# Optimization experiments

Hardware: AMD Instinct MI355X
Metric: run time of the kernel (lower is better)

The kernel has to match this reference:

```python
import jax, jax.numpy as jnp
import numpy as np

N_EMBD = 1024
N_HEAD = 16
HEAD_DIM = N_EMBD // N_HEAD


def setup_inputs() -> dict:
    key = jax.random.key(0)
    k1, k2, k3, k4, k5 = jax.random.split(key, 5)
    B, T, C = 4, 2048, N_EMBD
    s = 1.0 / np.sqrt(C)
    return {
        "x": jax.random.normal(k1, (B, T, C), dtype=jnp.float32),
        "W_attn": jax.random.normal(k2, (C, 3 * C), dtype=jnp.float32) * s,
        "b_attn": jnp.zeros((3 * C,), dtype=jnp.float32),
        "W_proj": jax.random.normal(k3, (C, C), dtype=jnp.float32) * s,
        "b_proj": jnp.zeros((C,), dtype=jnp.float32),
    }


def reference(x, W_attn, b_attn, W_proj, b_proj):
    B, T, C = x.shape
    H, D = N_HEAD, HEAD_DIM
    # fused QKV projection
    qkv = x @ W_attn + b_attn                       # [B,T,3C]
    q, k, v = jnp.split(qkv, 3, axis=2)
    q = q.reshape(B, T, H, D).transpose(0, 2, 1, 3)  # [B,H,T,D]
    k = k.reshape(B, T, H, D).transpose(0, 2, 1, 3)
    v = v.reshape(B, T, H, D).transpose(0, 2, 1, 3)
    # causal scaled dot-product attention
    scale = 1.0 / jnp.sqrt(jnp.asarray(D, dtype=x.dtype))
    scores = jnp.einsum('bhqd,bhkd->bhqk', q, k) * scale  # [B,H,T,T]
    causal = jnp.tril(jnp.ones((T, T), dtype=bool))
    scores = jnp.where(causal[None, None], scores, jnp.finfo(x.dtype).min)
    attn = jax.nn.softmax(scores, axis=-1)
    y = jnp.einsum('bhqk,bhkd->bhqd', attn, v)      # [B,H,T,D]
    y = y.transpose(0, 2, 1, 3).reshape(B, T, C)
    return y @ W_proj + b_proj
```

## Files before the change

kernel.cpp:

```cpp
#include <hip/hip_runtime.h>
#include <hip/hip_bf16.h>
#include <cstdint>

#define B_ 4
#define T_ 2048
#define C_ 1024
#define H_ 16
#define D_ 64
#define M_ (B_*T_)
#define N3 (3*C_)

typedef __bf16 bf16;
typedef __bf16 bf16x8 __attribute__((ext_vector_type(8)));
typedef __bf16 bf16x4 __attribute__((ext_vector_type(4)));
typedef float  floatx4 __attribute__((ext_vector_type(4)));

__device__ __forceinline__ void gl_lds16(const bf16* g, bf16* l) {
  __builtin_amdgcn_global_load_lds(
      (__attribute__((address_space(1))) void*)(void*)g,
      (__attribute__((address_space(3))) void*)(void*)l,
      16, 0, 0);
}

__device__ __forceinline__ uint32_t pack_bf16_trunc(float lo, float hi) {
  union { float f; uint32_t u; } a, b;
  a.f = lo; b.f = hi;
  return (a.u >> 16) | (b.u & 0xffff0000u);
}

__global__ void cast_to_bf16(const float* __restrict__ in, bf16* __restrict__ out, int n) {
  int i = (blockIdx.x * blockDim.x + threadIdx.x) * 4;
  if (i < n) {
    const float4 f = *(const float4*)(in + i);
    bf16x4 o;
    o.x = (bf16)f.x; o.y = (bf16)f.y; o.z = (bf16)f.z; o.w = (bf16)f.w;
    *(bf16x4*)(out + i) = o;
  }
}

__global__ void transpose_cast(const float* __restrict__ in, bf16* __restrict__ out,
                               int R, int C) {
  __shared__ float tile[32][33];
  int r0 = blockIdx.y * 32, c0 = blockIdx.x * 32;
  int tx = threadIdx.x & 31, ty = threadIdx.x >> 5;
  #pragma unroll
  for (int j = 0; j < 32; j += 8)
    tile[ty + j][tx] = in[(size_t)(r0 + ty + j) * C + c0 + tx];
  __syncthreads();
  #pragma unroll
  for (int j = 0; j < 32; j += 8)
    out[(size_t)(c0 + ty + j) * R + r0 + tx] = (bf16)tile[tx][ty + j];
}

__global__ __launch_bounds__(256)
void transpose_v(const bf16* __restrict__ in, bf16* __restrict__ out) {
  __shared__ __attribute__((aligned(16))) bf16 tileN[64 * 64];
  const int tid = threadIdx.x;
  const int bh = blockIdx.z;
  const int t0 = blockIdx.x * 64;
  const int sk = tid >> 2, scc = tid & 3;
  {
    const bf16* p = in + ((size_t)bh * T_ + t0 + sk) * D_ + scc * 16;
    const bf16x8 r0 = *(const bf16x8*)p;
    const bf16x8 r1 = *(const bf16x8*)(p + 8);
    *(bf16x8*)(tileN + sk * 64 + ((2 * scc)     ^ (sk & 7)) * 8) = r0;
    *(bf16x8*)(tileN + sk * 64 + ((2 * scc + 1) ^ (sk & 7)) * 8) = r1;
  }
  __syncthreads();
  const int tc = (tid & 7) * 8;
  #pragma unroll
  for (int half = 0; half < 2; half++) {
    const int d = (tid >> 3) + half * 32;
    bf16x8 o;
    #pragma unroll
    for (int j = 0; j < 8; j++) {
      const int slot = tc + j;
      const int row = 16 * (slot & 3) + (slot >> 2);
      o[j] = tileN[row * 64 + (((d >> 3) ^ (row & 7)) * 8) + (d & 7)];
    }
    *(bf16x8*)(out + ((size_t)bh * D_ + d) * T_ + t0 + tc) = o;
  }
}

template<int MODE>
__global__ __launch_bounds__(256)
void gemm_bt(const bf16* __restrict__ A, const bf16* __restrict__ Bt,
             const float* __restrict__ bias, float* __restrict__ out,
             bf16* __restrict__ qo, bf16* __restrict__ ko, bf16* __restrict__ vo,
             int M, int N, int K)
{
  __shared__ __attribute__((aligned(16))) bf16 As[128 * 32];
  __shared__ __attribute__((aligned(16))) bf16 Bs[128 * 32];

  const int tid  = threadIdx.x;
  const int w    = tid >> 6;
  const int lane = tid & 63;
  const int quad = lane >> 4;
  const int l16  = lane & 15;
  const int wm   = w & 1, wn = w >> 1;
  const int m0   = blockIdx.y * 128, n0 = blockIdx.x * 128;

  floatx4 acc[4][4] = {};

  const int lrow = lane >> 2;
  const int lk   = (lane & 3) * 8;

  const bf16* aptr = A  + (size_t)(m0 + w * 32 + lrow) * K + lk;
  const bf16* bptr = Bt + (size_t)(n0 + w * 32 + lrow) * K + lk;
  bf16* asl = As + w * 1024;
  bf16* bsl = Bs + w * 1024;

  for (int k0 = 0; k0 < K; k0 += 32) {
    gl_lds16(aptr,          asl);
    gl_lds16(aptr + 16 * K, asl + 512);
    gl_lds16(bptr,          bsl);
    gl_lds16(bptr + 16 * K, bsl + 512);
    aptr += 32; bptr += 32;
    __syncthreads();

    bf16x8 af[4], bfb[4];
    #pragma unroll
    for (int i = 0; i < 4; i++)
      af[i] = *(const bf16x8*)(As + (wm * 64 + i * 16 + l16) * 32 + quad * 8);
    #pragma unroll
    for (int i = 0; i < 4; i++)
      bfb[i] = *(const bf16x8*)(Bs + (wn * 64 + i * 16 + l16) * 32 + quad * 8);
    #pragma unroll
    for (int mi = 0; mi < 4; mi++)
      #pragma unroll
      for (int ni = 0; ni < 4; ni++)
        acc[mi][ni] = __builtin_amdgcn_mfma_f32_16x16x32_bf16(af[mi], bfb[ni], acc[mi][ni], 0, 0, 0);
    __syncthreads();
  }

  #pragma unroll
  for (int mi = 0; mi < 4; mi++) {
    #pragma unroll
    for (int ni = 0; ni < 4; ni++) {
      const int col = n0 + wn * 64 + ni * 16 + l16;
      const float bv = bias[col];
      #pragma unroll
      for (int r = 0; r < 4; r++) {
        const int row = m0 + wm * 64 + mi * 16 + quad * 4 + r;
        const float val = acc[mi][ni][r] + bv;
        if (MODE == 0) {
          const int b = row >> 11, t = row & 2047;
          const int s = col >> 10, c = col & 1023;
          const int h = c >> 6,  d = c & 63;
          bf16* dst = (s == 0) ? qo : (s == 1) ? ko : vo;
          dst[((size_t)(b * H_ + h) * T_ + t) * D_ + d] = (bf16)val;
        } else {
          out[(size_t)row * N + col] = val;
        }
      }
    }
  }
}


__device__ __forceinline__ void stage8(const bf16* g, int K, bf16* lds, int lane) {
  const int r = lane >> 3, s = (lane & 7) ^ r;
  gl_lds16(g + (size_t)r * K + s * 8, lds);
}
__device__ __forceinline__ void stage_half(const bf16* g, int K, bf16* lds, int wv, int lane) {
  stage8(g + (size_t)(wv * 16) * K,     K, lds + (wv * 16) * 64, lane);
  stage8(g + (size_t)(wv * 16 + 8) * K, K, lds + (wv * 16 + 8) * 64, lane);
}

#define GBAR asm volatile("s_barrier" ::: "memory")

template<int MODE>
__global__ __launch_bounds__(512, 2)
void gemm256(const bf16* __restrict__ A, const bf16* __restrict__ Bt,
             const float* __restrict__ bias, float* __restrict__ out,
             bf16* __restrict__ qo, bf16* __restrict__ ko, bf16* __restrict__ vo,
             int M, int N, int K)
{
  __shared__ __attribute__((aligned(16))) bf16 As[2][256 * 64];
  __shared__ __attribute__((aligned(16))) bf16 Bs[2][256 * 64];

  const int tid  = threadIdx.x;
  const int wv   = tid >> 6, lane = tid & 63;
  const int quad = lane >> 4, l16 = lane & 15;
  const int wm   = wv >> 2, wn = wv & 3;
  const int n0   = blockIdx.x * 256, m0 = blockIdx.y * 256;
  const int NTT  = K >> 6;

  floatx4 acc[8][4] = {};

  const bf16* Abase = A  + (size_t)m0 * K;
  const bf16* Bbase = Bt + (size_t)n0 * K;

  stage_half(Abase,                  K, As[0],            wv, lane);
  stage_half(Abase + (size_t)128*K,  K, As[0] + 128 * 64, wv, lane);
  stage_half(Bbase,                  K, Bs[0],            wv, lane);
  stage_half(Bbase + (size_t)128*K,  K, Bs[0] + 128 * 64, wv, lane);
  stage_half(Bbase + 64,             K, Bs[1],            wv, lane);
  stage_half(Abase + 64,             K, As[1],            wv, lane);
  asm volatile("s_waitcnt vmcnt(4)" ::: "memory");
  GBAR;

#define LOADA(qm)                                                          \
  _Pragma("unroll")                                                        \
  for (int mi = 0; mi < 4; mi++) {                                         \
    const int row = wm * 128 + (qm) * 64 + mi * 16 + l16;                  \
    const bf16* rp = bufA + row * 64;                                      \
    af[mi][0] = *(const bf16x8*)(rp + (( quad      ^ (row & 7)) * 8));     \
    af[mi][1] = *(const bf16x8*)(rp + (((4 | quad) ^ (row & 7)) * 8));     \
  }
#define LOADB(qn)                                                          \
  _Pragma("unroll")                                                        \
  for (int ni = 0; ni < 2; ni++) {                                         \
    const int row = wn * 64 + (qn) * 32 + ni * 16 + l16;                   \
    const bf16* rp = bufB + row * 64;                                      \
    bfr[(qn)*2+ni][0] = *(const bf16x8*)(rp + (( quad      ^ (row & 7)) * 8)); \
    bfr[(qn)*2+ni][1] = *(const bf16x8*)(rp + (((4 | quad) ^ (row & 7)) * 8)); \
  }
#define MM(qm, qn)                                                         \
  __builtin_amdgcn_s_setprio(1);                                           \
  _Pragma("unroll")                                                        \
  for (int mi = 0; mi < 4; mi++)                                           \
    _Pragma("unroll")                                                      \
    for (int ni = 0; ni < 2; ni++) {                                       \
      acc[(qm)*4+mi][(qn)*2+ni] = __builtin_amdgcn_mfma_f32_16x16x32_bf16( \
          af[mi][0], bfr[(qn)*2+ni][0], acc[(qm)*4+mi][(qn)*2+ni], 0, 0, 0); \
      acc[(qm)*4+mi][(qn)*2+ni] = __builtin_amdgcn_mfma_f32_16x16x32_bf16( \
          af[mi][1], bfr[(qn)*2+ni][1], acc[(qm)*4+mi][(qn)*2+ni], 0, 0, 0); \
    }                                                                      \
  __builtin_amdgcn_s_setprio(0);

  #pragma unroll 1
  for (int t = 0; t < NTT; t++) {
    const int cur = t & 1;
    const bf16* bufA = As[cur];
    const bf16* bufB = Bs[cur];
    bf16* nA = As[cur ^ 1];
    bf16* nB = Bs[cur ^ 1];
    bf16* cA = As[cur];
    bf16* cB = Bs[cur];
    const int kn1 = (t + 1) * 64, kn2 = (t + 2) * 64;
    const bool h1 = (t + 1 < NTT), h2 = (t + 2 < NTT);

    bf16x8 af[4][2], bfr[4][2];

    LOADA(0);
    LOADB(0);
    if (h1) stage_half(Abase + (size_t)128 * K + kn1, K, nA + 128 * 64, wv, lane);
    GBAR;
    MM(0, 0);
    GBAR;

    LOADB(1);
    if (h1) stage_half(Bbase + (size_t)128 * K + kn1, K, nB + 128 * 64, wv, lane);
    GBAR;
    MM(0, 1);
    GBAR;

    LOADA(1);
    if (h2) stage_half(Bbase + kn2, K, cB, wv, lane);
    GBAR;
    MM(1, 0);
    GBAR;

    if (h2) stage_half(Abase + kn2, K, cA, wv, lane);
    GBAR;
    MM(1, 1);
    asm volatile("s_waitcnt vmcnt(4)" ::: "memory");
    GBAR;
  }

#undef LOADA
#undef LOADB
#undef MM

  #pragma unroll
  for (int mi8 = 0; mi8 < 8; mi8++) {
    #pragma unroll
    for (int nf = 0; nf < 4; nf++) {
      const int col = n0 + wn * 64 + nf * 16 + l16;
      const float bv = bias[col];
      #pragma unroll
      for (int r = 0; r < 4; r++) {
        const int row = m0 + wm * 128 + mi8 * 16 + quad * 4 + r;
        const float val = acc[mi8][nf][r] + bv;
        if (MODE == 0) {
          const int b = row >> 11, tt = row & 2047;
          const int s = col >> 10, c = col & 1023;
          const int h = c >> 6, d = c & 63;
          bf16* dst = (s == 0) ? qo : (s == 1) ? ko : vo;
          dst[((size_t)(b * H_ + h) * T_ + tt) * D_ + d] = (bf16)val;
        } else {
          out[(size_t)row * N + col] = val;
        }
      }
    }
  }
}

__global__ __launch_bounds__(256)
void attn_kernel(const bf16* __restrict__ Q, const bf16* __restrict__ Kp,
                 const bf16* __restrict__ Vtp, bf16* __restrict__ Y)
{
  __shared__ __attribute__((aligned(16))) bf16 Ks[2][64 * 72];
  __shared__ __attribute__((aligned(16))) bf16 Vs[2][64 * 72];
  __shared__ __attribute__((aligned(16))) bf16 Ps[4][16 * 72];

  const int tid  = threadIdx.x;
  const int w    = tid >> 6, lane = tid & 63;
  const int quad = lane >> 4, l16 = lane & 15;
  const int bh = blockIdx.x;
  const int b = bh >> 4, h = bh & 15;
  const int pr = blockIdx.y;

  const int sk = tid >> 2;
  const int sc = (tid & 3) * 16;

  const float SC = 0.125f * 1.44269504088896f;

  #pragma unroll 1
  for (int sel = 0; sel < 2; sel++) {
    const int qt = sel ? pr : 15 - pr;
    const int q0 = qt * 128;
    const int nch = 2 * qt + 2;

    bf16x8 qf[2][2];
    #pragma unroll
    for (int mt = 0; mt < 2; mt++) {
      const bf16* qp = Q + ((size_t)bh * T_ + q0 + mt * 64 + w * 16 + l16) * D_ + quad * 8;
      qf[mt][0] = *(const bf16x8*)qp;
      qf[mt][1] = *(const bf16x8*)(qp + 32);
    }

    floatx4 o[2][4] = {};
    float l_r[2][4] = {};

    const bf16* kpp = Kp  + (size_t)bh * T_ * D_ + (size_t)sk * D_ + sc;
    const bf16* vpp = Vtp + (size_t)bh * D_ * T_ + (size_t)sk * T_ + sc;

    {
      const bf16x8 k0 = *(const bf16x8*)kpp, k1 = *(const bf16x8*)(kpp + 8);
      const bf16x8 v0 = *(const bf16x8*)vpp, v1 = *(const bf16x8*)(vpp + 8);
      bf16* kd = Ks[0] + sk * 72 + sc;
      *(bf16x8*)kd = k0; *(bf16x8*)(kd + 8) = k1;
      bf16* vd = Vs[0] + sk * 72 + sc;
      *(bf16x8*)vd = v0; *(bf16x8*)(vd + 8) = v1;
      kpp += 64 * D_; vpp += 64;
    }
    __syncthreads();

    #pragma unroll 1
    for (int c = 0; c < nch; c++) {
      const int cur = c & 1;

      bf16x8 nk0, nk1, nv0, nv1;
      const bool have = (c + 1 < nch);
      if (have) {
        nk0 = *(const bf16x8*)kpp; nk1 = *(const bf16x8*)(kpp + 8);
        nv0 = *(const bf16x8*)vpp; nv1 = *(const bf16x8*)(vpp + 8);
        kpp += 64 * D_; vpp += 64;
      }

      const bf16* KsC = Ks[cur];
      const bf16* VsC = Vs[cur];
      const int kv0 = c * 64;
      const bool act0 = (c < nch - 1);

      floatx4 s[2][4];
      #pragma unroll
      for (int nt = 0; nt < 4; nt++) {
        const bf16x8 kf0 = *(const bf16x8*)(KsC + (nt * 16 + l16) * 72 + quad * 8);
        const bf16x8 kf1 = *(const bf16x8*)(KsC + (nt * 16 + l16) * 72 + 32 + quad * 8);
        if (act0) {
          floatx4 z = {};
          z = __builtin_amdgcn_mfma_f32_16x16x32_bf16(qf[0][0], kf0, z, 0, 0, 0);
          s[0][nt] = __builtin_amdgcn_mfma_f32_16x16x32_bf16(qf[0][1], kf1, z, 0, 0, 0);
        }
        floatx4 z = {};
        z = __builtin_amdgcn_mfma_f32_16x16x32_bf16(qf[1][0], kf0, z, 0, 0, 0);
        s[1][nt] = __builtin_amdgcn_mfma_f32_16x16x32_bf16(qf[1][1], kf1, z, 0, 0, 0);
      }

      bf16x8 vfr[4][2];
      #pragma unroll
      for (int nt = 0; nt < 4; nt++) {
        vfr[nt][0] = *(const bf16x8*)(VsC + (nt * 16 + l16) * 72 + quad * 8);
        vfr[nt][1] = *(const bf16x8*)(VsC + (nt * 16 + l16) * 72 + 32 + quad * 8);
      }

      #pragma unroll
      for (int mt = 0; mt < 2; mt++) {
        if (mt == 0 && !act0) continue;
        const bool diag = (c == 2 * qt + mt);
        #pragma unroll
        for (int r = 0; r < 4; r++) {
          const int qrow = q0 + mt * 64 + w * 16 + quad * 4 + r;
          float x0 = s[mt][0][r], x1 = s[mt][1][r], x2 = s[mt][2][r], x3 = s[mt][3][r];
          if (diag) {
            if (kv0      + l16 > qrow) x0 = -1e30f;
            if (kv0 + 16 + l16 > qrow) x1 = -1e30f;
            if (kv0 + 32 + l16 > qrow) x2 = -1e30f;
            if (kv0 + 48 + l16 > qrow) x3 = -1e30f;
          }
          const float e0 = __builtin_amdgcn_exp2f(fmaf(x0, SC, -8.f));
          const float e1 = __builtin_amdgcn_exp2f(fmaf(x1, SC, -8.f));
          const float e2 = __builtin_amdgcn_exp2f(fmaf(x2, SC, -8.f));
          const float e3 = __builtin_amdgcn_exp2f(fmaf(x3, SC, -8.f));
          l_r[mt][r] += (e0 + e1) + (e2 + e3);
          uint2 pk;
          pk.x = pack_bf16_trunc(e0, e1);
          pk.y = pack_bf16_trunc(e2, e3);
          *(uint2*)(&Ps[w][(quad * 4 + r) * 72 + l16 * 4]) = pk;
        }
        const bf16x8 pf0 = *(const bf16x8*)(&Ps[w][l16 * 72 + quad * 8]);
        const bf16x8 pf1 = *(const bf16x8*)(&Ps[w][l16 * 72 + 32 + quad * 8]);
        #pragma unroll
        for (int nt = 0; nt < 4; nt++) {
          o[mt][nt] = __builtin_amdgcn_mfma_f32_16x16x32_bf16(pf0, vfr[nt][0], o[mt][nt], 0, 0, 0);
          o[mt][nt] = __builtin_amdgcn_mfma_f32_16x16x32_bf16(pf1, vfr[nt][1], o[mt][nt], 0, 0, 0);
        }
      }

      if (have) {
        bf16* kd = Ks[cur ^ 1] + sk * 72 + sc;
        *(bf16x8*)kd = nk0; *(bf16x8*)(kd + 8) = nk1;
        bf16* vd = Vs[cur ^ 1] + sk * 72 + sc;
        *(bf16x8*)vd = nv0; *(bf16x8*)(vd + 8) = nv1;
      }
      __syncthreads();
    }

    #pragma unroll
    for (int mt = 0; mt < 2; mt++) {
      #pragma unroll
      for (int r = 0; r < 4; r++) {
        float ls = l_r[mt][r];
        ls += __shfl_xor(ls, 1);
        ls += __shfl_xor(ls, 2);
        ls += __shfl_xor(ls, 4);
        ls += __shfl_xor(ls, 8);
        const float inv = 1.f / ls;
        const int t = q0 + mt * 64 + w * 16 + quad * 4 + r;
        #pragma unroll
        for (int nt = 0; nt < 4; nt++)
          Y[((size_t)b * T_ + t) * C_ + h * D_ + nt * 16 + l16] = (bf16)(o[mt][nt][r] * inv);
      }
    }
  }
}

extern "C" void kernel_launch(void* const* d_in, const int* in_sizes, int n_in,
                              void* d_out, int out_size, void* d_ws, size_t ws_size,
                              hipStream_t stream)
{
  const float* x      = (const float*)d_in[0];
  const float* W_attn = (const float*)d_in[1];
  const float* b_attn = (const float*)d_in[2];
  const float* W_proj = (const float*)d_in[3];
  const float* b_proj = (const float*)d_in[4];
  float* out = (float*)d_out;

  bf16* xb  = (bf16*)d_ws;
  bf16* wat = xb  + (size_t)M_ * C_;
  bf16* wpt = wat + (size_t)N3 * C_;
  bf16* qb  = wpt + (size_t)C_ * C_;
  bf16* kb  = qb  + (size_t)M_ * C_;
  bf16* vb  = kb  + (size_t)M_ * C_;
  bf16* yb  = vb  + (size_t)M_ * C_;
  bf16* vtb = xb;

  cast_to_bf16<<<dim3(M_ * C_ / 1024), 256, 0, stream>>>(x, xb, M_ * C_);
  transpose_cast<<<dim3(N3 / 32, C_ / 32), 256, 0, stream>>>(W_attn, wat, C_, N3);
  transpose_cast<<<dim3(C_ / 32, C_ / 32), 256, 0, stream>>>(W_proj, wpt, C_, C_);
  gemm256<0><<<dim3(N3 / 256, M_ / 256), 512, 0, stream>>>(
      xb, wat, b_attn, nullptr, qb, kb, vb, M_, N3, C_);
  transpose_v<<<dim3(T_ / 64, 1, B_ * H_), 256, 0, stream>>>(vb, vtb);
  attn_kernel<<<dim3(B_ * H_, 8), 256, 0, stream>>>(qb, kb, vtb, yb);
  gemm_bt<1><<<dim3(C_ / 128, M_ / 128), 256, 0, stream>>>(
      yb, wpt, b_proj, out, nullptr, nullptr, nullptr, M_, C_, C_);
}
```

Baseline: 270.0 us.

## Keep attention probabilities in registers by computing transposed scores

Swaps the MFMA operand order so the score tile comes out transposed (keys along rows, queries along lanes), which lets the exponentiated probabilities be packed directly into the A-operand layout for the PV MFMA instead of round-tripping through a per-wave LDS buffer. The V-transpose kernel's row permutation is adjusted to match the new key ordering within the packed fragments. Row-sum reduction changes to cross-quad shuffles plus a lane shuffle to redistribute the reciprocal. This removes LDS writes and reads per chunk, at the risk of subtle layout mismatches in the permutation.

```diff
diff --git a/kernel.cpp b/kernel.cpp
--- a/kernel.cpp
+++ b/kernel.cpp
@@ -75,7 +75,8 @@
     #pragma unroll
     for (int j = 0; j < 8; j++) {
       const int slot = tc + j;
-      const int row = 16 * (slot & 3) + (slot >> 2);
+      const int row = (slot & 3) + 4 * ((slot >> 3) & 3) + 16 * ((slot >> 2) & 1)
+                    + 32 * (slot >> 5);
       o[j] = tileN[row * 64 + (((d >> 3) ^ (row & 7)) * 8) + (d & 7)];
     }
     *(bf16x8*)(out + ((size_t)bh * D_ + d) * T_ + t0 + tc) = o;
@@ -156,7 +157,6 @@
     }
   }
 }
-
 
 __device__ __forceinline__ void stage8(const bf16* g, int K, bf16* lds, int lane) {
   const int r = lane >> 3, s = (lane & 7) ^ r;
@@ -303,7 +303,6 @@
 {
   __shared__ __attribute__((aligned(16))) bf16 Ks[2][64 * 72];
   __shared__ __attribute__((aligned(16))) bf16 Vs[2][64 * 72];
-  __shared__ __attribute__((aligned(16))) bf16 Ps[4][16 * 72];
 
   const int tid  = threadIdx.x;
   const int w    = tid >> 6, lane = tid & 63;
@@ -332,7 +331,7 @@
     }
 
     floatx4 o[2][4] = {};
-    float l_r[2][4] = {};
+    float l_r[2] = {0.f, 0.f};
 
     const bf16* kpp = Kp  + (size_t)bh * T_ * D_ + (size_t)sk * D_ + sc;
     const bf16* vpp = Vtp + (size_t)bh * D_ * T_ + (size_t)sk * T_ + sc;
@@ -372,12 +371,12 @@
         const bf16x8 kf1 = *(const bf16x8*)(KsC + (nt * 16 + l16) * 72 + 32 + quad * 8);
         if (act0) {
           floatx4 z = {};
-          z = __builtin_amdgcn_mfma_f32_16x16x32_bf16(qf[0][0], kf0, z, 0, 0, 0);
-          s[0][nt] = __builtin_amdgcn_mfma_f32_16x16x32_bf16(qf[0][1], kf1, z, 0, 0, 0);
+          z = __builtin_amdgcn_mfma_f32_16x16x32_bf16(kf0, qf[0][0], z, 0, 0, 0);
+          s[0][nt] = __builtin_amdgcn_mfma_f32_16x16x32_bf16(kf1, qf[0][1], z, 0, 0, 0);
         }
         floatx4 z = {};
-        z = __builtin_amdgcn_mfma_f32_16x16x32_bf16(qf[1][0], kf0, z, 0, 0, 0);
-        s[1][nt] = __builtin_amdgcn_mfma_f32_16x16x32_bf16(qf[1][1], kf1, z, 0, 0, 0);
+        z = __builtin_amdgcn_mfma_f32_16x16x32_bf16(kf0, qf[1][0], z, 0, 0, 0);
+        s[1][nt] = __builtin_amdgcn_mfma_f32_16x16x32_bf16(kf1, qf[1][1], z, 0, 0, 0);
       }
 
       bf16x8 vfr[4][2];
@@ -391,32 +390,36 @@
       for (int mt = 0; mt < 2; mt++) {
         if (mt == 0 && !act0) continue;
         const bool diag = (c == 2 * qt + mt);
-        #pragma unroll
-        for (int r = 0; r < 4; r++) {
-          const int qrow = q0 + mt * 64 + w * 16 + quad * 4 + r;
-          float x0 = s[mt][0][r], x1 = s[mt][1][r], x2 = s[mt][2][r], x3 = s[mt][3][r];
-          if (diag) {
-            if (kv0      + l16 > qrow) x0 = -1e30f;
-            if (kv0 + 16 + l16 > qrow) x1 = -1e30f;
-            if (kv0 + 32 + l16 > qrow) x2 = -1e30f;
-            if (kv0 + 48 + l16 > qrow) x3 = -1e30f;
-          }
-          const float e0 = __builtin_amdgcn_exp2f(fmaf(x0, SC, -8.f));
-          const float e1 = __builtin_amdgcn_exp2f(fmaf(x1, SC, -8.f));
-          const float e2 = __builtin_amdgcn_exp2f(fmaf(x2, SC, -8.f));
-          const float e3 = __builtin_amdgcn_exp2f(fmaf(x3, SC, -8.f));
-          l_r[mt][r] += (e0 + e1) + (e2 + e3);
-          uint2 pk;
-          pk.x = pack_bf16_trunc(e0, e1);
-          pk.y = pack_bf16_trunc(e2, e3);
-          *(uint2*)(&Ps[w][(quad * 4 + r) * 72 + l16 * 4]) = pk;
-        }
-        const bf16x8 pf0 = *(const bf16x8*)(&Ps[w][l16 * 72 + quad * 8]);
-        const bf16x8 pf1 = *(const bf16x8*)(&Ps[w][l16 * 72 + 32 + quad * 8]);
+        const int qrow = q0 + mt * 64 + w * 16 + l16;
+        float e[4][4];
+        float ls0 = 0.f, ls1 = 0.f;
         #pragma unroll
         for (int nt = 0; nt < 4; nt++) {
-          o[mt][nt] = __builtin_amdgcn_mfma_f32_16x16x32_bf16(pf0, vfr[nt][0], o[mt][nt], 0, 0, 0);
-          o[mt][nt] = __builtin_amdgcn_mfma_f32_16x16x32_bf16(pf1, vfr[nt][1], o[mt][nt], 0, 0, 0);
+          #pragma unroll
+          for (int r = 0; r < 4; r++) {
+            float x = s[mt][nt][r];
+            if (diag) {
+              if (kv0 + nt * 16 + quad * 4 + r > qrow) x = -1e30f;
+            }
+            const float ev = __builtin_amdgcn_exp2f(fmaf(x, SC, -8.f));
+            e[nt][r] = ev;
+            if (nt & 1) ls1 += ev; else ls0 += ev;
+          }
+        }
+        l_r[mt] += ls0 + ls1;
+
+        union { uint32_t u[4]; bf16x8 v; } pa0, pa1;
+        #pragma unroll
+        for (int jj = 0; jj < 4; jj++) {
+          pa0.u[jj] = pack_bf16_trunc(e[(jj >> 1)][(jj & 1) * 2],
+                                      e[(jj >> 1)][(jj & 1) * 2 + 1]);
+          pa1.u[jj] = pack_bf16_trunc(e[2 + (jj >> 1)][(jj & 1) * 2],
+                                      e[2 + (jj >> 1)][(jj & 1) * 2 + 1]);
+        }
+        #pragma unroll
+        for (int nt = 0; nt < 4; nt++) {
+          o[mt][nt] = __builtin_amdgcn_mfma_f32_16x16x32_bf16(pa0.v, vfr[nt][0], o[mt][nt], 0, 0, 0);
+          o[mt][nt] = __builtin_amdgcn_mfma_f32_16x16x32_bf16(pa1.v, vfr[nt][1], o[mt][nt], 0, 0, 0);
         }
       }
 
@@ -431,14 +434,13 @@
 
     #pragma unroll
     for (int mt = 0; mt < 2; mt++) {
+      float ls = l_r[mt];
+      ls += __shfl_xor(ls, 16);
+      ls += __shfl_xor(ls, 32);
+      const float invls = 1.f / ls;
       #pragma unroll
       for (int r = 0; r < 4; r++) {
-        float ls = l_r[mt][r];
-        ls += __shfl_xor(ls, 1);
-        ls += __shfl_xor(ls, 2);
-        ls += __shfl_xor(ls, 4);
-        ls += __shfl_xor(ls, 8);
-        const float inv = 1.f / ls;
+        const float inv = __shfl(invls, (lane & 48) + quad * 4 + r);
         const int t = q0 + mt * 64 + w * 16 + quad * 4 + r;
         #pragma unroll
         for (int nt = 0; nt < 4; nt++)
```

Measured after the change: 272.2 us. About the same (+0.8%).
